# Kernel optimization log

Measured on AMD Instinct MI355X. Metric: run time of the kernel, lower is better.

## Reference

```python
import jax, jax.numpy as jnp
import numpy as np

N, E = 50000, 800000
F_IN, HID, HEADS, NCLS = 128, 64, 4, 16
NEG_SLOPE = 0.2


def setup_inputs() -> dict:
    key = jax.random.key(0)
    ks = jax.random.split(key, 16)
    def glorot(k, shape):
        fan_in, fan_out = shape[0], shape[-1]
        lim = jnp.sqrt(6.0 / (fan_in + fan_out))
        return jax.random.uniform(k, shape, jnp.float32, -lim, lim)
    x = jax.random.normal(ks[0], (N, F_IN), jnp.float32)
    edge_index = jax.random.randint(ks[1], (2, E), 0, N, dtype=jnp.int64)
    inp = {"x": x, "edge_index": edge_index}
    # layer 1: F_IN -> HID x HEADS (concat)
    inp["W1"] = glorot(ks[2], (F_IN, HEADS * HID))
    inp["a1_src"] = glorot(ks[3], (HEADS, HID))
    inp["a1_dst"] = glorot(ks[4], (HEADS, HID))
    inp["b1"] = jnp.zeros((HEADS * HID,), jnp.float32)
    # layer 2: HEADS*HID -> HID x HEADS (concat)
    inp["W2"] = glorot(ks[5], (HEADS * HID, HEADS * HID))
    inp["a2_src"] = glorot(ks[6], (HEADS, HID))
    inp["a2_dst"] = glorot(ks[7], (HEADS, HID))
    inp["b2"] = jnp.zeros((HEADS * HID,), jnp.float32)
    # layer 3: HEADS*HID -> NCLS, heads=1, concat=False (mean)
    inp["W3"] = glorot(ks[8], (HEADS * HID, NCLS))
    inp["a3_src"] = glorot(ks[9], (1, NCLS))
    inp["a3_dst"] = glorot(ks[10], (1, NCLS))
    inp["b3"] = jnp.zeros((NCLS,), jnp.float32)
    return inp


def gat_conv(x, src, dst, W, a_src, a_dst, b, heads, out_dim, concat):
    n = x.shape[0]
    h = (x @ W).reshape(n, heads, out_dim)           # [N, H, D]
    s_src = jnp.sum(h * a_src, axis=-1)              # [N, H]
    s_dst = jnp.sum(h * a_dst, axis=-1)              # [N, H]
    e = jax.nn.leaky_relu(s_src[src] + s_dst[dst], NEG_SLOPE)  # [E, H]
    # segment softmax over incoming edges of each dst node
    m = jax.ops.segment_max(e, dst, num_segments=n)
    ex = jnp.exp(e - m[dst])
    z = jax.ops.segment_sum(ex, dst, num_segments=n)
    alpha = ex / z[dst]                              # [E, H]
    msg = h[src] * alpha[:, :, None]                 # [E, H, D]
    out = jax.ops.segment_sum(msg, dst, num_segments=n)  # [N, H, D]
    out = out.reshape(n, heads * out_dim) if concat else out.mean(axis=1)
    return out + b


def reference(x, edge_index, W1, a1_src, a1_dst, b1, W2, a2_src, a2_dst, b2,
              W3, a3_src, a3_dst, b3):
    n = x.shape[0]
    loop = jnp.arange(n, dtype=edge_index.dtype)
    src = jnp.concatenate([edge_index[0], loop])     # add self-loops (PyG default)
    dst = jnp.concatenate([edge_index[1], loop])
    h = jax.nn.elu(gat_conv(x, src, dst, W1, a1_src, a1_dst, b1, HEADS, HID, True))
    h = jax.nn.elu(gat_conv(h, src, dst, W2, a2_src, a2_dst, b2, HEADS, HID, True))
    h = gat_conv(h, src, dst, W3, a3_src, a3_dst, b3, 1, NCLS, False)
    return jax.nn.log_softmax(h, axis=1)
```

## Files before the change

kernel.cpp:

```cpp
#include <hip/hip_runtime.h>
#include <hip/hip_bf16.h>
#include <math.h>

#define N_NODES 50000
#define N_EDGES 800000
#define F_IN    128
#define HID     64
#define HEADS   4
#define NCLS    16
#define NEG_SLOPE 0.2f

typedef __attribute__((ext_vector_type(8))) _Float16 half8v;
typedef __attribute__((ext_vector_type(4))) float f32x4;
typedef __attribute__((ext_vector_type(2))) float f32x2;

static __device__ __forceinline__ float lrelu(float x) {
    return x >= 0.f ? x : NEG_SLOPE * x;
}
static __device__ __forceinline__ unsigned short f2h(float f) {
    _Float16 h = (_Float16)f;
    return __builtin_bit_cast(unsigned short, h);
}
static __device__ __forceinline__ float h2f(unsigned short u) {
    return (float)__builtin_bit_cast(_Float16, u);
}

__global__ void k_zero(int4* __restrict__ p, int n4) {
    int i = blockIdx.x * blockDim.x + threadIdx.x;
    if (i < n4) p[i] = int4{0, 0, 0, 0};
}

#define NB_WT1  128
#define NB_WT2  256
#define NB_HIST 3125
__global__ void k_prep(const float* __restrict__ W1, unsigned short* __restrict__ W1t,
                       const float* __restrict__ W2, unsigned short* __restrict__ W2t,
                       const int* __restrict__ dst, int* __restrict__ counts,
                       unsigned short* __restrict__ rank) {
    int bid = blockIdx.x, tid = threadIdx.x;
    if (bid < NB_WT1) {
        int i = bid * 256 + tid;
        int k = i >> 8, c = i & 255;
        W1t[c * F_IN + k] = f2h(W1[i]);
    } else if (bid < NB_WT1 + NB_WT2) {
        int i = (bid - NB_WT1) * 256 + tid;
        int k = i >> 8, c = i & 255;
        W2t[c * 256 + k] = f2h(W2[i]);
    } else {
        int i = (bid - NB_WT1 - NB_WT2) * 256 + tid;
        if (i < N_EDGES) rank[i] = (unsigned short)atomicAdd(&counts[dst[i]], 1);
    }
}

__global__ __launch_bounds__(256) void k_scan1(const int* __restrict__ counts, int* __restrict__ incl,
                                               int* __restrict__ bsums, int n) {
    __shared__ int wsum[4];
    int blk = blockIdx.x, tid = threadIdx.x;
    int lane = tid & 63, w = tid >> 6;
    int i0 = blk * 1024 + tid * 4;
    int v[4];
    #pragma unroll
    for (int j = 0; j < 4; j++) v[j] = (i0 + j < n) ? counts[i0 + j] : 0;
    int t = v[0] + v[1] + v[2] + v[3];
    int x = t;
    #pragma unroll
    for (int d = 1; d < 64; d <<= 1) { int y = __shfl_up(x, d); if (lane >= d) x += y; }
    if (lane == 63) wsum[w] = x;
    __syncthreads();
    int woff = 0;
    #pragma unroll
    for (int ww = 0; ww < 4; ww++) woff += (ww < w) ? wsum[ww] : 0;
    int p = woff + x - t;
    #pragma unroll
    for (int j = 0; j < 4; j++) { p += v[j]; if (i0 + j < n) incl[i0 + j] = p; }
    if (tid == 255) bsums[blk] = woff + x;
}

__global__ void k_scan2(const int* __restrict__ bsums, int* __restrict__ boffs, int nb, int* rowptr_end) {
    int lane = threadIdx.x;
    int v = (lane < nb) ? bsums[lane] : 0;
    int x = v;
    #pragma unroll
    for (int d = 1; d < 64; d <<= 1) { int y = __shfl_up(x, d); if (lane >= d) x += y; }
    if (lane < nb) boffs[lane] = x - v;
    if (lane == 63) *rowptr_end = x;
}

__global__ void k_scan3(const int* __restrict__ incl, const int* __restrict__ counts,
                        const int* __restrict__ boffs, int* __restrict__ rowptr, int n) {
    int i = blockIdx.x * blockDim.x + threadIdx.x;
    if (i < n) rowptr[i] = boffs[i >> 10] + incl[i] - counts[i];
}

static __device__ __forceinline__ int swz(int r, int lc) {
    return r * 4 + (lc ^ (r & 3) ^ ((r >> 2) & 1));
}

template<int CONVA>
static __device__ __forceinline__ void gemm_body(
        int bid, const void* __restrict__ Av, const unsigned short* __restrict__ Bt,
        const float* __restrict__ asrc, const float* __restrict__ adst,
        unsigned char* __restrict__ C8, float* __restrict__ s_src, float* __restrict__ s_dst,
        int M, int K, unsigned short* Asm, unsigned short* Bsm) {
    int tid = threadIdx.x;
    int lane = tid & 63, wid = tid >> 6;
    int bx = bid & 1, by = bid >> 1;
    int row0 = by * 128, col0 = bx * 128;
    int wr = wid >> 1, wc = wid & 1;
    f32x4 acc[4][4] = {};

    for (int k0 = 0; k0 < K; k0 += 32) {
        __syncthreads();
        #pragma unroll
        for (int s = 0; s < 2; s++) {
            int c = tid + s * 256;
            int row = c >> 2, lc = c & 3;
            int gr = row0 + row; if (gr >= M) gr = 0;
            uint4 va;
            if (CONVA) {
                const float* Af = (const float*)Av + (size_t)gr * K + k0 + lc * 8;
                float4 fa = *(const float4*)Af;
                float4 fb = *(const float4*)(Af + 4);
                va.x = (unsigned)f2h(fa.x) | ((unsigned)f2h(fa.y) << 16);
                va.y = (unsigned)f2h(fa.z) | ((unsigned)f2h(fa.w) << 16);
                va.z = (unsigned)f2h(fb.x) | ((unsigned)f2h(fb.y) << 16);
                va.w = (unsigned)f2h(fb.z) | ((unsigned)f2h(fb.w) << 16);
            } else {
                va = *(const uint4*)((const unsigned short*)Av + (size_t)gr * K + k0 + lc * 8);
            }
            *(uint4*)(&Asm[swz(row, lc) * 8]) = va;
            uint4 vb = *(const uint4*)(Bt + (size_t)(col0 + row) * K + k0 + lc * 8);
            *(uint4*)(&Bsm[swz(row, lc) * 8]) = vb;
        }
        __syncthreads();
        half8v af[4], bg[4];
        int lq = lane >> 4;
        #pragma unroll
        for (int m = 0; m < 4; m++) {
            int r = wr * 64 + m * 16 + (lane & 15);
            af[m] = *(const half8v*)(&Asm[swz(r, lq) * 8]);
        }
        #pragma unroll
        for (int n = 0; n < 4; n++) {
            int r = wc * 64 + n * 16 + (lane & 15);
            bg[n] = *(const half8v*)(&Bsm[swz(r, lq) * 8]);
        }
        #pragma unroll
        for (int m = 0; m < 4; m++)
            #pragma unroll
            for (int n = 0; n < 4; n++)
                acc[m][n] = __builtin_amdgcn_mfma_f32_16x16x32_f16(af[m], bg[n], acc[m][n], 0, 0, 0);
    }

    #pragma unroll
    for (int m = 0; m < 4; m++) {
        #pragma unroll
        for (int r = 0; r < 4; r++) {
            int row = row0 + wr * 64 + m * 16 + (lane >> 4) * 4 + r;
            if (row < M) {
                int q01 = __builtin_amdgcn_cvt_pk_fp8_f32(acc[m][0][r], acc[m][1][r], 0, false);
                int q23 = __builtin_amdgcn_cvt_pk_fp8_f32(acc[m][2][r], acc[m][3][r], 0, false);
                size_t base = (size_t)row * 256 + col0 + wc * 64 + (lane & 15);
                C8[base]      = (unsigned char)(q01 & 0xff);
                C8[base + 16] = (unsigned char)((q01 >> 8) & 0xff);
                C8[base + 32] = (unsigned char)(q23 & 0xff);
                C8[base + 48] = (unsigned char)((q23 >> 8) & 0xff);
            }
        }
    }

    int c16 = lane & 15, lq = lane >> 4;
    int head = bx * 2 + wc;
    float avs[4], avd[4];
    #pragma unroll
    for (int nn = 0; nn < 4; nn++) {
        avs[nn] = asrc[head * 64 + nn * 16 + c16];
        avd[nn] = adst[head * 64 + nn * 16 + c16];
    }
    #pragma unroll
    for (int mm = 0; mm < 4; mm++) {
        #pragma unroll
        for (int r = 0; r < 4; r++) {
            float ps = 0.f, pd = 0.f;
            #pragma unroll
            for (int nn = 0; nn < 4; nn++) {
                ps += acc[mm][nn][r] * avs[nn];
                pd += acc[mm][nn][r] * avd[nn];
            }
            #pragma unroll
            for (int off = 1; off < 16; off <<= 1) {
                ps += __shfl_xor(ps, off);
                pd += __shfl_xor(pd, off);
            }
            if (c16 == 0) {
                int grow = row0 + wr * 64 + mm * 16 + lq * 4 + r;
                if (grow < M) {
                    s_src[grow * 4 + head] = ps;
                    s_dst[grow * 4 + head] = pd;
                }
            }
        }
    }
}

__global__ __launch_bounds__(256) void k_gemm_mfma(const unsigned short* __restrict__ A,
                                                   const unsigned short* __restrict__ Bt,
                                                   const float* __restrict__ asrc,
                                                   const float* __restrict__ adst,
                                                   unsigned char* __restrict__ C8,
                                                   float* __restrict__ s_src,
                                                   float* __restrict__ s_dst,
                                                   int M, int K) {
    __shared__ unsigned short Asm[128 * 32];
    __shared__ unsigned short Bsm[128 * 32];
    gemm_body<0>(blockIdx.x, A, Bt, asrc, adst, C8, s_src, s_dst, M, K, Asm, Bsm);
}

__global__ __launch_bounds__(256) void k_b(const float* __restrict__ A,
                                           const unsigned short* __restrict__ Bt,
                                           const float* __restrict__ asrc,
                                           const float* __restrict__ adst,
                                           unsigned char* __restrict__ C8,
                                           float* __restrict__ s_src,
                                           float* __restrict__ s_dst,
                                           int M, int K, int gemmBlocks,
                                           const int* __restrict__ src, const int* __restrict__ dst,
                                           const int* __restrict__ rowptr,
                                           const unsigned short* __restrict__ rank,
                                           unsigned* __restrict__ colp, int e) {
    __shared__ unsigned short Asm[128 * 32];
    __shared__ unsigned short Bsm[128 * 32];
    int bid = blockIdx.x;
    if (bid < gemmBlocks) {
        gemm_body<1>(bid, A, Bt, asrc, adst, C8, s_src, s_dst, M, K, Asm, Bsm);
    } else {
        int half = (e + 1) >> 1;
        int i = (bid - gemmBlocks) * 256 + (int)threadIdx.x;
        if (i < half) {
            int d = dst[i];
            colp[rowptr[d] + rank[i]] = (unsigned)src[i] | ((unsigned)d << 16);
        }
        int j = i + half;
        if (j < e) {
            int d = dst[j];
            colp[rowptr[d] + rank[j]] = (unsigned)src[j] | ((unsigned)d << 16);
        }
    }
}

__global__ void k_aggregate(const unsigned char* __restrict__ h8, const int* __restrict__ rowptr,
                            const unsigned* __restrict__ colp,
                            const float* __restrict__ s_src, const float* __restrict__ s_dst,
                            const float* __restrict__ bias,
                            unsigned short* __restrict__ out, int n, int e) {
    int wave = (blockIdx.x * blockDim.x + threadIdx.x) >> 6;
    int lane = threadIdx.x & 63;
    if (wave >= n) return;
    int half = lane >> 5, l5 = lane & 31;
    int head = l5 >> 3;
    int j8 = l5 & 7;
    int base8 = lane & ~7;
    unsigned foff = (unsigned)(l5 * 8);
    int rs = rowptr[wave], re = rowptr[wave + 1];
    float sd = s_dst[wave * 4 + head];

    float z = 0.f;
    f32x2 a01 = {0.f, 0.f}, a23 = {0.f, 0.f}, a45 = {0.f, 0.f}, a67 = {0.f, 0.f};
    #define PEDGE(SV) __expf(fminf(lrelu((SV) + sd), 80.f))
    #define ACC8(P, HV) { \
        f32x2 pbc = {(P), (P)}; \
        f32x2 v0 = __builtin_amdgcn_cvt_pk_f32_fp8((HV).x, false); \
        f32x2 v1 = __builtin_amdgcn_cvt_pk_f32_fp8((HV).x, true);  \
        f32x2 v2 = __builtin_amdgcn_cvt_pk_f32_fp8((HV).y, false); \
        f32x2 v3 = __builtin_amdgcn_cvt_pk_f32_fp8((HV).y, true);  \
        asm("v_pk_fma_f32 %0, %1, %2, %0" : "+v"(a01) : "v"(v0), "v"(pbc)); \
        asm("v_pk_fma_f32 %0, %1, %2, %0" : "+v"(a23) : "v"(v1), "v"(pbc)); \
        asm("v_pk_fma_f32 %0, %1, %2, %0" : "+v"(a45) : "v"(v2), "v"(pbc)); \
        asm("v_pk_fma_f32 %0, %1, %2, %0" : "+v"(a67) : "v"(v3), "v"(pbc)); \
        z += (P); }

    if (half == 0) {
        float pself = PEDGE(s_src[wave * 4 + head]);
        uint2 own = *(const uint2*)(h8 + (((unsigned)wave << 8) + foff));
        ACC8(pself, own);
    }
    int i = rs + half;
    for (; i + 14 < re; i += 16) {
        unsigned cc[8];
        #pragma unroll
        for (int j = 0; j < 8; j++) cc[j] = colp[i + 2 * j];
        float s_own = s_src[(cc[j8] & 0xffffu) * 4 + head];
        uint2 hv[8];
        #pragma unroll
        for (int j = 0; j < 8; j++)
            hv[j] = *(const uint2*)(h8 + (((cc[j] & 0xffffu) << 8) + foff));
        float p_own = PEDGE(s_own);
        float pv[8];
        #pragma unroll
        for (int j = 0; j < 8; j++) pv[j] = __shfl(p_own, base8 + j);
        #pragma unroll
        for (int j = 0; j < 8; j++) { ACC8(pv[j], hv[j]); }
    }
    for (; i + 6 < re; i += 8) {
        unsigned cc[4];
        #pragma unroll
        for (int j = 0; j < 4; j++) cc[j] = colp[i + 2 * j];
        float s_own = s_src[(cc[j8 & 3] & 0xffffu) * 4 + head];
        uint2 hv[4];
        #pragma unroll
        for (int j = 0; j < 4; j++)
            hv[j] = *(const uint2*)(h8 + (((cc[j] & 0xffffu) << 8) + foff));
        float p_own = PEDGE(s_own);
        float pv[4];
        #pragma unroll
        for (int j = 0; j < 4; j++) pv[j] = __shfl(p_own, base8 + j);
        #pragma unroll
        for (int j = 0; j < 4; j++) { ACC8(pv[j], hv[j]); }
    }
    for (; i < re; i += 2) {
        unsigned c0 = colp[i];
        float s0 = s_src[(c0 & 0xffffu) * 4 + head];
        uint2 h0 = *(const uint2*)(h8 + (((c0 & 0xffffu) << 8) + foff));
        float p0 = PEDGE(s0);
        ACC8(p0, h0);
    }
    #undef ACC8
    #undef PEDGE
    z += __shfl_xor(z, 32);
    float a[8] = {a01.x, a01.y, a23.x, a23.y, a45.x, a45.y, a67.x, a67.y};
    #pragma unroll
    for (int j = 0; j < 8; j++) a[j] += __shfl_xor(a[j], 32);

    if (half == 0) {
        float inv = 1.f / z;
        int f0 = l5 * 8;
        float4 bv0 = *(const float4*)(bias + f0);
        float4 bv1 = *(const float4*)(bias + f0 + 4);
        float o[8];
        o[0] = a[0] * inv + bv0.x; o[1] = a[1] * inv + bv0.y;
        o[2] = a[2] * inv + bv0.z; o[3] = a[3] * inv + bv0.w;
        o[4] = a[4] * inv + bv1.x; o[5] = a[5] * inv + bv1.y;
        o[6] = a[6] * inv + bv1.z; o[7] = a[7] * inv + bv1.w;
        #pragma unroll
        for (int j = 0; j < 8; j++) o[j] = o[j] > 0.f ? o[j] : __expf(o[j]) - 1.f;
        uint4 ov;
        unsigned* w = (unsigned*)&ov;
        #pragma unroll
        for (int j = 0; j < 4; j++)
            w[j] = (unsigned)f2h(o[2 * j]) | ((unsigned)f2h(o[2 * j + 1]) << 16);
        *(uint4*)(out + (size_t)wave * 256 + f0) = ov;
    }
}

__global__ __launch_bounds__(256) void k_gemm3(const unsigned short* __restrict__ A,
                                               const float* __restrict__ B,
                                               const float* __restrict__ a3s,
                                               const float* __restrict__ a3d,
                                               unsigned short* __restrict__ C,
                                               float* __restrict__ s_src,
                                               float* __restrict__ s_dst,
                                               int M, int K) {
    __shared__ float Bs[256 * 16];
    for (int i = threadIdx.x; i < K * 16; i += 256) Bs[i] = B[i];
    __syncthreads();
    int tx = threadIdx.x & 15;
    int ty = threadIdx.x >> 4;
    int row = blockIdx.x * 16 + ty;
    if (row >= M) return;
    const unsigned short* Ar = A + (size_t)row * K;
    float acc = 0.f;
    for (int kk = 0; kk < K; kk += 8) {
        uint4 va = *(const uint4*)(Ar + kk);
        const unsigned* u = (const unsigned*)&va;
        #pragma unroll
        for (int j = 0; j < 4; j++) {
            float lo = h2f((unsigned short)(u[j] & 0xffff));
            float hi = h2f((unsigned short)(u[j] >> 16));
            acc += lo * Bs[(kk + 2 * j) * 16 + tx] + hi * Bs[(kk + 2 * j + 1) * 16 + tx];
        }
    }
    C[(size_t)row * 16 + tx] = f2h(acc);
    float ps = acc * a3s[tx], pd = acc * a3d[tx];
    #pragma unroll
    for (int off = 1; off < 16; off <<= 1) {
        ps += __shfl_xor(ps, off);
        pd += __shfl_xor(pd, off);
    }
    if (tx == 0) { s_src[row] = ps; s_dst[row] = pd; }
}

__global__ void k_agg3(const unsigned short* __restrict__ h3, const int* __restrict__ rowptr,
                       const unsigned* __restrict__ colp,
                       const float* __restrict__ s_src, const float* __restrict__ s_dst,
                       const float* __restrict__ b3,
                       float* __restrict__ outp, int n) {
    int wave = (blockIdx.x * blockDim.x + threadIdx.x) >> 6;
    int lane = threadIdx.x & 63;
    if (wave >= n) return;
    int g = lane >> 4, c = lane & 15;
    int rs = rowptr[wave], re = rowptr[wave + 1];
    float sdn = s_dst[wave];

    float z = 0.f, acc = 0.f;
    if (g == 0) {
        float p = __expf(fminf(lrelu(s_src[wave] + sdn), 80.f));
        z += p;
        acc += p * h2f(h3[(size_t)wave * 16 + c]);
    }
    int i = rs + g;
    for (; i + 12 < re; i += 16) {
        int s0 = colp[i] & 0xffff,     s1 = colp[i + 4] & 0xffff;
        int s2 = colp[i + 8] & 0xffff, s3 = colp[i + 12] & 0xffff;
        float q0 = s_src[s0], q1 = s_src[s1], q2 = s_src[s2], q3 = s_src[s3];
        float v0 = h2f(h3[(size_t)s0 * 16 + c]), v1 = h2f(h3[(size_t)s1 * 16 + c]);
        float v2 = h2f(h3[(size_t)s2 * 16 + c]), v3 = h2f(h3[(size_t)s3 * 16 + c]);
        float p0 = __expf(fminf(lrelu(q0 + sdn), 80.f));
        float p1 = __expf(fminf(lrelu(q1 + sdn), 80.f));
        float p2 = __expf(fminf(lrelu(q2 + sdn), 80.f));
        float p3 = __expf(fminf(lrelu(q3 + sdn), 80.f));
        z += (p0 + p1) + (p2 + p3);
        acc += p0 * v0 + p1 * v1 + p2 * v2 + p3 * v3;
    }
    for (; i + 4 < re; i += 8) {
        int s0 = colp[i] & 0xffff, s1 = colp[i + 4] & 0xffff;
        float q0 = s_src[s0], q1 = s_src[s1];
        float v0 = h2f(h3[(size_t)s0 * 16 + c]), v1 = h2f(h3[(size_t)s1 * 16 + c]);
        float p0 = __expf(fminf(lrelu(q0 + sdn), 80.f));
        float p1 = __expf(fminf(lrelu(q1 + sdn), 80.f));
        z += p0 + p1;
        acc += p0 * v0 + p1 * v1;
    }
    for (; i < re; i += 4) {
        int s = colp[i] & 0xffff;
        float p = __expf(fminf(lrelu(s_src[s] + sdn), 80.f));
        z += p;
        acc += p * h2f(h3[(size_t)s * 16 + c]);
    }
    z += __shfl_xor(z, 16);  z += __shfl_xor(z, 32);
    acc += __shfl_xor(acc, 16); acc += __shfl_xor(acc, 32);
    if (lane < 16) {
        float v = acc / z + b3[c];
        float mm = v;
        #pragma unroll
        for (int off = 1; off < 16; off <<= 1) mm = fmaxf(mm, __shfl_xor(mm, off));
        float se = __expf(v - mm);
        #pragma unroll
        for (int off = 1; off < 16; off <<= 1) se += __shfl_xor(se, off);
        outp[(size_t)wave * 16 + c] = v - mm - logf(se);
    }
}

extern "C" void kernel_launch(void* const* d_in, const int* in_sizes, int n_in,
                              void* d_out, int out_size, void* d_ws, size_t ws_size,
                              hipStream_t stream) {
    const float* x      = (const float*)d_in[0];
    const int*   ei     = (const int*)d_in[1];
    const float* W1     = (const float*)d_in[2];
    const float* a1_src = (const float*)d_in[3];
    const float* a1_dst = (const float*)d_in[4];
    const float* b1     = (const float*)d_in[5];
    const float* W2     = (const float*)d_in[6];
    const float* a2_src = (const float*)d_in[7];
    const float* a2_dst = (const float*)d_in[8];
    const float* b2     = (const float*)d_in[9];
    const float* W3     = (const float*)d_in[10];
    const float* a3_src = (const float*)d_in[11];
    const float* a3_dst = (const float*)d_in[12];
    const float* b3     = (const float*)d_in[13];
    float* outp = (float*)d_out;

    const int N = N_NODES, E = N_EDGES;
    const int* src = ei;
    const int* dst = ei + E;

    char* ws = (char*)d_ws;
    size_t off = 0;
    auto alloc = [&](size_t bytes) {
        void* p = ws + off;
        off = (off + bytes + 255) & ~(size_t)255;
        return p;
    };
    int*   rowptr = (int*)alloc((N + 1) * sizeof(int));
    int*   counts = (int*)alloc(N * sizeof(int));
    unsigned* colp = (unsigned*)alloc(E * sizeof(unsigned));
    unsigned short* rank = (unsigned short*)alloc(E * sizeof(short));
    int*   incl   = (int*)alloc(N * sizeof(int));
    int*   bsums  = (int*)alloc(64 * sizeof(int));
    int*   boffs  = (int*)alloc(64 * sizeof(int));
    float* s_src  = (float*)alloc((size_t)N * HEADS * sizeof(float));
    float* s_dst  = (float*)alloc((size_t)N * HEADS * sizeof(float));
    unsigned short* W1t = (unsigned short*)alloc((size_t)256 * F_IN * sizeof(short));
    unsigned short* W2t = (unsigned short*)alloc((size_t)256 * 256 * sizeof(short));
    unsigned char* hA8  = (unsigned char*)alloc((size_t)N * 256);
    unsigned short* hB  = (unsigned short*)alloc((size_t)N * 256 * sizeof(short));
    unsigned short* h3  = (unsigned short*)alloc((size_t)N * 16 * sizeof(short));
    (void)ws_size;

    const int aggBlocks = (N + 3) / 4;
    const int gemmBlocks = ((N + 127) / 128) * 2;
    const int scatBlocks = ((E + 1) / 2 + 255) / 256;

    k_zero<<<(N / 4 + 255) / 256, 256, 0, stream>>>((int4*)counts, N / 4);
    k_prep<<<NB_WT1 + NB_WT2 + NB_HIST, 256, 0, stream>>>(W1, W1t, W2, W2t, dst, counts, rank);

    const int nb = (N + 1023) / 1024;
    k_scan1<<<nb, 256, 0, stream>>>(counts, incl, bsums, N);
    k_scan2<<<1, 64, 0, stream>>>(bsums, boffs, nb, rowptr + N);
    k_scan3<<<(N + 255) / 256, 256, 0, stream>>>(incl, counts, boffs, rowptr, N);

    k_b<<<gemmBlocks + scatBlocks, 256, 0, stream>>>(x, W1t, a1_src, a1_dst, hA8, s_src, s_dst,
                                                     N, F_IN, gemmBlocks,
                                                     src, dst, rowptr, rank, colp, E);
    k_aggregate<<<aggBlocks, 256, 0, stream>>>(hA8, rowptr, colp, s_src, s_dst, b1, hB, N, E);
    k_gemm_mfma<<<gemmBlocks, 256, 0, stream>>>(hB, W2t, a2_src, a2_dst, hA8, s_src, s_dst, N, 256);
    k_aggregate<<<aggBlocks, 256, 0, stream>>>(hA8, rowptr, colp, s_src, s_dst, b2, hB, N, E);
    k_gemm3<<<(N + 15) / 16, 256, 0, stream>>>(hB, W3, a3_src, a3_dst, h3, s_src, s_dst, N, 256);
    k_agg3<<<aggBlocks, 256, 0, stream>>>(h3, rowptr, colp, s_src, s_dst, b3, outp, N);
}
```

Before: 229.8 us.

## Shrink CSR column array to 16-bit and give each half-wave its own node

The packed 32-bit src|dst column entries become 16-bit source indices, which halves CSR index traffic in the scatter and in all three aggregation passes. The layer-1/2 aggregation now maps two destination nodes per wave, one per 32-lane half, instead of splitting one node's edges across the halves. This removes the cross-half shuffle reduction and the idle half during the epilogue, but the two halves may see unequal degrees and diverge. k_agg3 also computes each edge's exponential once and shares it through shuffles instead of every lane recomputing it.

```diff
diff --git a/kernel.cpp b/kernel.cpp
--- a/kernel.cpp
+++ b/kernel.cpp
@@ -227,7 +227,7 @@
                                            const int* __restrict__ src, const int* __restrict__ dst,
                                            const int* __restrict__ rowptr,
                                            const unsigned short* __restrict__ rank,
-                                           unsigned* __restrict__ colp, int e) {
+                                           unsigned short* __restrict__ col, int e) {
     __shared__ unsigned short Asm[128 * 32];
     __shared__ unsigned short Bsm[128 * 32];
     int bid = blockIdx.x;
@@ -238,31 +238,32 @@
         int i = (bid - gemmBlocks) * 256 + (int)threadIdx.x;
         if (i < half) {
             int d = dst[i];
-            colp[rowptr[d] + rank[i]] = (unsigned)src[i] | ((unsigned)d << 16);
+            col[rowptr[d] + rank[i]] = (unsigned short)src[i];
         }
         int j = i + half;
         if (j < e) {
             int d = dst[j];
-            colp[rowptr[d] + rank[j]] = (unsigned)src[j] | ((unsigned)d << 16);
+            col[rowptr[d] + rank[j]] = (unsigned short)src[j];
         }
     }
 }
 
 __global__ void k_aggregate(const unsigned char* __restrict__ h8, const int* __restrict__ rowptr,
-                            const unsigned* __restrict__ colp,
+                            const unsigned short* __restrict__ col,
                             const float* __restrict__ s_src, const float* __restrict__ s_dst,
                             const float* __restrict__ bias,
-                            unsigned short* __restrict__ out, int n, int e) {
+                            unsigned short* __restrict__ out, int n) {
     int wave = (blockIdx.x * blockDim.x + threadIdx.x) >> 6;
     int lane = threadIdx.x & 63;
-    if (wave >= n) return;
     int half = lane >> 5, l5 = lane & 31;
+    int node = wave * 2 + half;
+    if (node >= n) return;
     int head = l5 >> 3;
     int j8 = l5 & 7;
     int base8 = lane & ~7;
     unsigned foff = (unsigned)(l5 * 8);
-    int rs = rowptr[wave], re = rowptr[wave + 1];
-    float sd = s_dst[wave * 4 + head];
+    int rs = rowptr[node], re = rowptr[node + 1];
+    float sd = s_dst[node * 4 + head];
 
     float z = 0.f;
     f32x2 a01 = {0.f, 0.f}, a23 = {0.f, 0.f}, a45 = {0.f, 0.f}, a67 = {0.f, 0.f};
@@ -279,21 +280,21 @@
         asm("v_pk_fma_f32 %0, %1, %2, %0" : "+v"(a67) : "v"(v3), "v"(pbc)); \
         z += (P); }
 
-    if (half == 0) {
-        float pself = PEDGE(s_src[wave * 4 + head]);
-        uint2 own = *(const uint2*)(h8 + (((unsigned)wave << 8) + foff));
+    {
+        float pself = PEDGE(s_src[node * 4 + head]);
+        uint2 own = *(const uint2*)(h8 + (((unsigned)node << 8) + foff));
         ACC8(pself, own);
     }
-    int i = rs + half;
-    for (; i + 14 < re; i += 16) {
+    int i = rs;
+    for (; i + 7 < re; i += 8) {
         unsigned cc[8];
         #pragma unroll
-        for (int j = 0; j < 8; j++) cc[j] = colp[i + 2 * j];
-        float s_own = s_src[(cc[j8] & 0xffffu) * 4 + head];
+        for (int j = 0; j < 8; j++) cc[j] = col[i + j];
+        float s_own = s_src[cc[j8] * 4 + head];
         uint2 hv[8];
         #pragma unroll
         for (int j = 0; j < 8; j++)
-            hv[j] = *(const uint2*)(h8 + (((cc[j] & 0xffffu) << 8) + foff));
+            hv[j] = *(const uint2*)(h8 + ((cc[j] << 8) + foff));
         float p_own = PEDGE(s_own);
         float pv[8];
         #pragma unroll
@@ -301,15 +302,15 @@
         #pragma unroll
         for (int j = 0; j < 8; j++) { ACC8(pv[j], hv[j]); }
     }
-    for (; i + 6 < re; i += 8) {
+    for (; i + 3 < re; i += 4) {
         unsigned cc[4];
         #pragma unroll
-        for (int j = 0; j < 4; j++) cc[j] = colp[i + 2 * j];
-        float s_own = s_src[(cc[j8 & 3] & 0xffffu) * 4 + head];
+        for (int j = 0; j < 4; j++) cc[j] = col[i + j];
+        float s_own = s_src[cc[j8 & 3] * 4 + head];
         uint2 hv[4];
         #pragma unroll
         for (int j = 0; j < 4; j++)
-            hv[j] = *(const uint2*)(h8 + (((cc[j] & 0xffffu) << 8) + foff));
+            hv[j] = *(const uint2*)(h8 + ((cc[j] << 8) + foff));
         float p_own = PEDGE(s_own);
         float pv[4];
         #pragma unroll
@@ -317,39 +318,33 @@
         #pragma unroll
         for (int j = 0; j < 4; j++) { ACC8(pv[j], hv[j]); }
     }
-    for (; i < re; i += 2) {
-        unsigned c0 = colp[i];
-        float s0 = s_src[(c0 & 0xffffu) * 4 + head];
-        uint2 h0 = *(const uint2*)(h8 + (((c0 & 0xffffu) << 8) + foff));
+    for (; i < re; i++) {
+        unsigned c0 = col[i];
+        float s0 = s_src[c0 * 4 + head];
+        uint2 h0 = *(const uint2*)(h8 + ((c0 << 8) + foff));
         float p0 = PEDGE(s0);
         ACC8(p0, h0);
     }
     #undef ACC8
     #undef PEDGE
-    z += __shfl_xor(z, 32);
-    float a[8] = {a01.x, a01.y, a23.x, a23.y, a45.x, a45.y, a67.x, a67.y};
-    #pragma unroll
-    for (int j = 0; j < 8; j++) a[j] += __shfl_xor(a[j], 32);
-
-    if (half == 0) {
-        float inv = 1.f / z;
-        int f0 = l5 * 8;
-        float4 bv0 = *(const float4*)(bias + f0);
-        float4 bv1 = *(const float4*)(bias + f0 + 4);
-        float o[8];
-        o[0] = a[0] * inv + bv0.x; o[1] = a[1] * inv + bv0.y;
-        o[2] = a[2] * inv + bv0.z; o[3] = a[3] * inv + bv0.w;
-        o[4] = a[4] * inv + bv1.x; o[5] = a[5] * inv + bv1.y;
-        o[6] = a[6] * inv + bv1.z; o[7] = a[7] * inv + bv1.w;
-        #pragma unroll
-        for (int j = 0; j < 8; j++) o[j] = o[j] > 0.f ? o[j] : __expf(o[j]) - 1.f;
-        uint4 ov;
-        unsigned* w = (unsigned*)&ov;
-        #pragma unroll
-        for (int j = 0; j < 4; j++)
-            w[j] = (unsigned)f2h(o[2 * j]) | ((unsigned)f2h(o[2 * j + 1]) << 16);
-        *(uint4*)(out + (size_t)wave * 256 + f0) = ov;
-    }
+
+    float inv = 1.f / z;
+    int f0 = l5 * 8;
+    float4 bv0 = *(const float4*)(bias + f0);
+    float4 bv1 = *(const float4*)(bias + f0 + 4);
+    float o[8];
+    o[0] = a01.x * inv + bv0.x; o[1] = a01.y * inv + bv0.y;
+    o[2] = a23.x * inv + bv0.z; o[3] = a23.y * inv + bv0.w;
+    o[4] = a45.x * inv + bv1.x; o[5] = a45.y * inv + bv1.y;
+    o[6] = a67.x * inv + bv1.z; o[7] = a67.y * inv + bv1.w;
+    #pragma unroll
+    for (int j = 0; j < 8; j++) o[j] = o[j] > 0.f ? o[j] : __expf(o[j]) - 1.f;
+    uint4 ov;
+    unsigned* w = (unsigned*)&ov;
+    #pragma unroll
+    for (int j = 0; j < 4; j++)
+        w[j] = (unsigned)f2h(o[2 * j]) | ((unsigned)f2h(o[2 * j + 1]) << 16);
+    *(uint4*)(out + (size_t)node * 256 + f0) = ov;
 }
 
 __global__ __launch_bounds__(256) void k_gemm3(const unsigned short* __restrict__ A,
@@ -390,7 +385,7 @@
 }
 
 __global__ void k_agg3(const unsigned short* __restrict__ h3, const int* __restrict__ rowptr,
-                       const unsigned* __restrict__ colp,
+                       const unsigned short* __restrict__ col,
                        const float* __restrict__ s_src, const float* __restrict__ s_dst,
                        const float* __restrict__ b3,
                        float* __restrict__ outp, int n) {
@@ -398,6 +393,7 @@
     int lane = threadIdx.x & 63;
     if (wave >= n) return;
     int g = lane >> 4, c = lane & 15;
+    int gbase = lane & ~15;
     int rs = rowptr[wave], re = rowptr[wave + 1];
     float sdn = s_dst[wave];
 
@@ -409,29 +405,22 @@
     }
     int i = rs + g;
     for (; i + 12 < re; i += 16) {
-        int s0 = colp[i] & 0xffff,     s1 = colp[i + 4] & 0xffff;
-        int s2 = colp[i + 8] & 0xffff, s3 = colp[i + 12] & 0xffff;
-        float q0 = s_src[s0], q1 = s_src[s1], q2 = s_src[s2], q3 = s_src[s3];
-        float v0 = h2f(h3[(size_t)s0 * 16 + c]), v1 = h2f(h3[(size_t)s1 * 16 + c]);
-        float v2 = h2f(h3[(size_t)s2 * 16 + c]), v3 = h2f(h3[(size_t)s3 * 16 + c]);
-        float p0 = __expf(fminf(lrelu(q0 + sdn), 80.f));
-        float p1 = __expf(fminf(lrelu(q1 + sdn), 80.f));
-        float p2 = __expf(fminf(lrelu(q2 + sdn), 80.f));
-        float p3 = __expf(fminf(lrelu(q3 + sdn), 80.f));
+        int ss[4];
+        #pragma unroll
+        for (int j = 0; j < 4; j++) ss[j] = col[i + 4 * j];
+        float q_own = s_src[ss[c & 3]];
+        float v0 = h2f(h3[(size_t)ss[0] * 16 + c]), v1 = h2f(h3[(size_t)ss[1] * 16 + c]);
+        float v2 = h2f(h3[(size_t)ss[2] * 16 + c]), v3 = h2f(h3[(size_t)ss[3] * 16 + c]);
+        float p_own = __expf(fminf(lrelu(q_own + sdn), 80.f));
+        float p0 = __shfl(p_own, gbase + 0);
+        float p1 = __shfl(p_own, gbase + 1);
+        float p2 = __shfl(p_own, gbase + 2);
+        float p3 = __shfl(p_own, gbase + 3);
         z += (p0 + p1) + (p2 + p3);
         acc += p0 * v0 + p1 * v1 + p2 * v2 + p3 * v3;
     }
-    for (; i + 4 < re; i += 8) {
-        int s0 = colp[i] & 0xffff, s1 = colp[i + 4] & 0xffff;
-        float q0 = s_src[s0], q1 = s_src[s1];
-        float v0 = h2f(h3[(size_t)s0 * 16 + c]), v1 = h2f(h3[(size_t)s1 * 16 + c]);
-        float p0 = __expf(fminf(lrelu(q0 + sdn), 80.f));
-        float p1 = __expf(fminf(lrelu(q1 + sdn), 80.f));
-        z += p0 + p1;
-        acc += p0 * v0 + p1 * v1;
-    }
     for (; i < re; i += 4) {
-        int s = colp[i] & 0xffff;
+        int s = col[i];
         float p = __expf(fminf(lrelu(s_src[s] + sdn), 80.f));
         z += p;
         acc += p * h2f(h3[(size_t)s * 16 + c]);
@@ -482,7 +471,7 @@
     };
     int*   rowptr = (int*)alloc((N + 1) * sizeof(int));
     int*   counts = (int*)alloc(N * sizeof(int));
-    unsigned* colp = (unsigned*)alloc(E * sizeof(unsigned));
+    unsigned short* col = (unsigned short*)alloc(E * sizeof(short));
     unsigned short* rank = (unsigned short*)alloc(E * sizeof(short));
     int*   incl   = (int*)alloc(N * sizeof(int));
     int*   bsums  = (int*)alloc(64 * sizeof(int));
@@ -496,7 +485,8 @@
     unsigned short* h3  = (unsigned short*)alloc((size_t)N * 16 * sizeof(short));
     (void)ws_size;
 
-    const int aggBlocks = (N + 3) / 4;
+    const int aggBlocks  = (N + 3) / 4;
+    const int aggBlocks2 = (N + 7) / 8;
     const int gemmBlocks = ((N + 127) / 128) * 2;
     const int scatBlocks = ((E + 1) / 2 + 255) / 256;
 
@@ -510,10 +500,10 @@
 
     k_b<<<gemmBlocks + scatBlocks, 256, 0, stream>>>(x, W1t, a1_src, a1_dst, hA8, s_src, s_dst,
                                                      N, F_IN, gemmBlocks,
-                                                     src, dst, rowptr, rank, colp, E);
-    k_aggregate<<<aggBlocks, 256, 0, stream>>>(hA8, rowptr, colp, s_src, s_dst, b1, hB, N, E);
+                                                     src, dst, rowptr, rank, col, E);
+    k_aggregate<<<aggBlocks2, 256, 0, stream>>>(hA8, rowptr, col, s_src, s_dst, b1, hB, N);
     k_gemm_mfma<<<gemmBlocks, 256, 0, stream>>>(hB, W2t, a2_src, a2_dst, hA8, s_src, s_dst, N, 256);
-    k_aggregate<<<aggBlocks, 256, 0, stream>>>(hA8, rowptr, colp, s_src, s_dst, b2, hB, N, E);
+    k_aggregate<<<aggBlocks2, 256, 0, stream>>>(hA8, rowptr, col, s_src, s_dst, b2, hB, N);
     k_gemm3<<<(N + 15) / 16, 256, 0, stream>>>(hB, W3, a3_src, a3_dst, h3, s_src, s_dst, N, 256);
-    k_agg3<<<aggBlocks, 256, 0, stream>>>(h3, rowptr, colp, s_src, s_dst, b3, outp, N);
-}
+    k_agg3<<<aggBlocks, 256, 0, stream>>>(h3, rowptr, col, s_src, s_dst, b3, outp, N);
+}
```

Result: faster. 222.1 us (-3.4%).
